# Performance work log

Measured on AMD Instinct MI355X. Metric: run time of the kernel, lower is better.

## Reference

```python
import jax, jax.numpy as jnp
import numpy as np

B, T, D, H = 1, 2048, 1024, 16
Dh = D // H
GSA_SCALE = 0.25
LN_EPS = 1e-5


def setup_inputs() -> dict:
    key = jax.random.key(0)
    ks = jax.random.split(key, 24)
    s = 0.02
    def W(k, din, dout):
        return jax.random.normal(k, (din, dout), jnp.float32) * s
    inp = dict(
        x=jax.random.normal(ks[0], (B, T, D), jnp.float32),
        mask=jnp.ones((B, T, T), jnp.bool_),
        # MultiHeadAttention params (linears[0..3] = q,k,v,o)
        mha_wq=W(ks[1], D, D), mha_bq=jnp.zeros((D,), jnp.float32),
        mha_wk=W(ks[2], D, D), mha_bk=jnp.zeros((D,), jnp.float32),
        mha_wv=W(ks[3], D, D), mha_bv=jnp.zeros((D,), jnp.float32),
        mha_wo=W(ks[4], D, D), mha_bo=jnp.zeros((D,), jnp.float32),
        # _GeodesicSelfAttention params
        gsa_wq=W(ks[5], D, D), gsa_bq=jnp.zeros((D,), jnp.float32),
        gsa_wk=W(ks[6], D, D), gsa_bk=jnp.zeros((D,), jnp.float32),
        gsa_wv=W(ks[7], D, D), gsa_bv=jnp.zeros((D,), jnp.float32),
        gsa_wo=W(ks[8], D, D), gsa_bo=jnp.zeros((D,), jnp.float32),
        log_diag=jnp.zeros((H, Dh), jnp.float32),  # nn.Parameter(torch.zeros(h, dk))
        # LayerNorms
        ln_mha_g=jnp.ones((D,), jnp.float32), ln_mha_b=jnp.zeros((D,), jnp.float32),
        ln_gsa_g=jnp.ones((D,), jnp.float32), ln_gsa_b=jnp.zeros((D,), jnp.float32),
        # mix scalar (initialized to -2.0 in __init__)
        gsa_mix=jnp.asarray(-2.0, jnp.float32),
        # gate: Linear(D,D) -> GELU -> Linear(D,1), last bias filled with 0.5
        gate_w1=W(ks[9], D, D), gate_b1=jnp.zeros((D,), jnp.float32),
        gate_w2=W(ks[10], D, 1), gate_b2=jnp.full((1,), 0.5, jnp.float32),
    )
    return inp


def _ln(x, g, b):
    m = x.mean(-1, keepdims=True)
    v = ((x - m) ** 2).mean(-1, keepdims=True)
    return (x - m) / jnp.sqrt(v + LN_EPS) * g + b


def _heads(y):  # [B,T,D] -> [B,H,T,Dh]
    return y.reshape(B, T, H, Dh).transpose(0, 2, 1, 3)


def _merge(y):  # [B,H,T,Dh] -> [B,T,D]
    return y.transpose(0, 2, 1, 3).reshape(B, T, D)


def _forward(x, mask, mha_wq, mha_bq, mha_wk, mha_bk, mha_wv, mha_bv, mha_wo, mha_bo,
             gsa_wq, gsa_bq, gsa_wk, gsa_bk, gsa_wv, gsa_bv, gsa_wo, gsa_bo,
             log_diag, ln_mha_g, ln_mha_b, ln_gsa_g, ln_gsa_b, gsa_mix,
             gate_w1, gate_b1, gate_w2, gate_b2):
    inv_sqrt_dh = 1.0 / jnp.sqrt(jnp.float32(Dh))
    m4 = mask[:, None, :, :]  # [B,1,T,T]

    # ---- standard MHA branch ----
    q = _heads(x @ mha_wq + mha_bq)
    k = _heads(x @ mha_wk + mha_bk)
    v = _heads(x @ mha_wv + mha_bv)
    scores = jnp.einsum('bhtd,bhsd->bhts', q, k) * inv_sqrt_dh
    scores = jnp.where(m4, scores, -jnp.inf)
    p = jax.nn.softmax(scores, axis=-1)
    mha_out = _merge(jnp.einsum('bhts,bhsd->bhtd', p, v)) @ mha_wo + mha_bo

    # ---- geodesic (Mahalanobis) branch ----
    qg = _heads(x @ gsa_wq + gsa_bq)
    kg = _heads(x @ gsa_wk + gsa_bk)
    vg = _heads(x @ gsa_wv + gsa_bv)
    diag = jax.nn.softplus(log_diag) + 1e-6          # [H,Dh]
    diag4 = diag[None, :, None, :]
    qM = qg * diag4
    q2M = (qg * qM).sum(-1)                           # [B,H,T]
    k2M = (kg * (kg * diag4)).sum(-1)                 # [B,H,T]
    cross = jnp.einsum('bhtd,bhsd->bhts', qM, kg)     # [B,H,T,T]
    dist = q2M[..., :, None] + k2M[..., None, :] - 2.0 * cross
    s = -0.5 * dist * inv_sqrt_dh
    s = jnp.where(m4, s, -jnp.inf)
    all_inf = jnp.all(jnp.isneginf(s), axis=-1, keepdims=True)
    s = jnp.where(all_inf, 0.0, s)
    pg = jax.nn.softmax(s * GSA_SCALE, axis=-1)
    gsa_out = _merge(jnp.einsum('bhts,bhsd->bhtd', pg, vg)) @ gsa_wo + gsa_bo

    # ---- gated mix ----
    mha_out = _ln(mha_out, ln_mha_g, ln_mha_b)
    gsa_out = jax.nn.sigmoid(gsa_mix) * _ln(gsa_out, ln_gsa_g, ln_gsa_b)
    g = jax.nn.gelu(x @ gate_w1 + gate_b1, approximate=False) @ gate_w2 + gate_b2
    alpha = 0.9 * jax.nn.sigmoid(g)                   # alpha_cap = 0.9, [B,T,1]
    return alpha * mha_out + (1.0 - alpha) * gsa_out


def reference(x, mask, mha_wq, mha_bq, mha_wk, mha_bk, mha_wv, mha_bv, mha_wo, mha_bo,
              gsa_wq, gsa_bq, gsa_wk, gsa_bk, gsa_wv, gsa_bv, gsa_wo, gsa_bo,
              log_diag, ln_mha_g, ln_mha_b, ln_gsa_g, ln_gsa_b, gsa_mix,
              gate_w1, gate_b1, gate_w2, gate_b2):
    return _forward(x, mask, mha_wq, mha_bq, mha_wk, mha_bk, mha_wv, mha_bv, mha_wo, mha_bo,
                    gsa_wq, gsa_bq, gsa_wk, gsa_bk, gsa_wv, gsa_bv, gsa_wo, gsa_bo,
                    log_diag, ln_mha_g, ln_mha_b, ln_gsa_g, ln_gsa_b, gsa_mix,
                    gate_w1, gate_b1, gate_w2, gate_b2)
```

## Files before the change

### kernel.cpp

```cpp
#include <hip/hip_runtime.h>
#include <stdint.h>

typedef unsigned short u16;
typedef u16   u16x4  __attribute__((ext_vector_type(4)));
typedef u16   u16x8  __attribute__((ext_vector_type(8)));
typedef __bf16 bf16x8 __attribute__((ext_vector_type(8)));
typedef float f32x4  __attribute__((ext_vector_type(4)));

#define SEQ   2048
#define DM    1024
#define NHEAD 16
#define DHEAD 64

#define QM_SCALE 0.180336880f
#define QG_SCALE 0.045084220f
#define K2_SCALE 0.022542110f

static __device__ __forceinline__ u16 f2b(float f) {
  uint32_t u = __float_as_uint(f);
  u += 0x7fffu + ((u >> 16) & 1u);
  return (u16)(u >> 16);
}
static __device__ __forceinline__ float b2f(u16 u) {
  return __uint_as_float(((uint32_t)u) << 16);
}

static __device__ __forceinline__ void gload16(const u16* g, u16* l) {
  __builtin_amdgcn_global_load_lds(
      (const __attribute__((address_space(1))) unsigned int*)g,
      (__attribute__((address_space(3))) unsigned int*)l, 16, 0, 0);
}

__global__ void precast_kernel(const float* __restrict__ x, u16* __restrict__ xb,
                               const float* __restrict__ log_diag, float* __restrict__ diag) {
  int i = blockIdx.x * 256 + threadIdx.x;
  if (i < SEQ * DM) xb[i] = f2b(x[i]);
  if (i < NHEAD * DHEAD) {
    float v = log_diag[i];
    float sp = (v > 20.f) ? v : log1pf(__expf(v));
    diag[i] = sp + 1e-6f;
  }
}

struct WTArgs { const float* w[9]; u16* o[9]; };

__global__ __launch_bounds__(256) void wtrans_kernel(WTArgs a) {
  const float* __restrict__ src = a.w[blockIdx.z];
  u16* __restrict__ dst = a.o[blockIdx.z];
  int r0 = blockIdx.y * 64, c0 = blockIdx.x * 64;
  __shared__ float tile[64][65];
  int tid = threadIdx.x;
  int r = tid >> 2, o8 = (tid & 3) * 16;
#pragma unroll
  for (int i = 0; i < 16; i += 4) {
    float4 v = *(const float4*)&src[(r0 + r) * DM + c0 + o8 + i];
    tile[r][o8 + i + 0] = v.x; tile[r][o8 + i + 1] = v.y;
    tile[r][o8 + i + 2] = v.z; tile[r][o8 + i + 3] = v.w;
  }
  __syncthreads();
  u16x8 w0, w1;
#pragma unroll
  for (int i = 0; i < 8; ++i) w0[i] = f2b(tile[o8 + i][r]);
#pragma unroll
  for (int i = 0; i < 8; ++i) w1[i] = f2b(tile[o8 + 8 + i][r]);
  *(u16x8*)&dst[(c0 + r) * DM + r0 + o8]     = w0;
  *(u16x8*)&dst[(c0 + r) * DM + r0 + o8 + 8] = w1;
}

struct GemmDesc { const u16* A; const u16* Bt; const float* bias; void* out;
                  int mode; int k0; int klen; float scale; };
struct GemmParams { GemmDesc d[8]; const float* diag; };

__global__ __launch_bounds__(256) void gemm_bt_kernel(GemmParams p) {
  GemmDesc g = p.d[blockIdx.z];
  const int K = DM;
  const int m0 = blockIdx.y * 128, n0 = blockIdx.x * 128;
  const int tid = threadIdx.x;
  const int wave = tid >> 6, lane = tid & 63, ln = lane & 15, quad = lane >> 4;
  const int wr = (wave >> 1) * 64, wc = (wave & 1) * 64;

  __shared__ __align__(16) u16 As[2 * 128 * 32];
  __shared__ __align__(16) u16 Bs[2 * 128 * 32];

  const f32x4 fz = {0.f, 0.f, 0.f, 0.f};
  f32x4 acc[4][4];
#pragma unroll
  for (int i = 0; i < 4; ++i)
#pragma unroll
    for (int j = 0; j < 4; ++j) acc[i][j] = fz;

  const u16* Aps[4]; const u16* Bps[4]; u16* dstA[4]; u16* dstB[4];
#pragma unroll
  for (int s = 0; s < 4; ++s) {
    int vr = s * 64 + wave * 16 + (lane >> 2);
    int c = vr >> 7, row = vr & 127;
    Aps[s] = g.A  + (size_t)(m0 + row) * K + g.k0 + c * 32 + (lane & 3) * 8;
    Bps[s] = g.Bt + (size_t)(n0 + row) * K + g.k0 + c * 32 + (lane & 3) * 8;
    dstA[s] = &As[s * 2048 + tid * 8];
    dstB[s] = &Bs[s * 2048 + tid * 8];
  }

  for (int kk = 0; kk < g.klen; kk += 64) {
#pragma unroll
    for (int s = 0; s < 4; ++s) {
      gload16(Aps[s] + kk, dstA[s]);
      gload16(Bps[s] + kk, dstB[s]);
    }
    __syncthreads();
#pragma unroll
    for (int c = 0; c < 2; ++c) {
      bf16x8 af[4], bfr[4];
#pragma unroll
      for (int mb = 0; mb < 4; ++mb)
        af[mb] = *(const bf16x8*)&As[c * 4096 + (wr + mb * 16 + ln) * 32 + quad * 8];
#pragma unroll
      for (int nb = 0; nb < 4; ++nb)
        bfr[nb] = *(const bf16x8*)&Bs[c * 4096 + (wc + nb * 16 + ln) * 32 + quad * 8];
#pragma unroll
      for (int mb = 0; mb < 4; ++mb)
#pragma unroll
        for (int nb = 0; nb < 4; ++nb)
          acc[mb][nb] = __builtin_amdgcn_mfma_f32_16x16x32_bf16(af[mb], bfr[nb], acc[mb][nb], 0, 0, 0);
    }
    __syncthreads();
  }

  const int mode = g.mode;
#pragma unroll
  for (int mb = 0; mb < 4; ++mb) {
    int row = m0 + wr + mb * 16 + quad * 4;
#pragma unroll
    for (int nb = 0; nb < 4; ++nb) {
      int col = n0 + wc + nb * 16 + ln;
      float bv = g.bias ? g.bias[col] : 0.f;
      f32x4 a = acc[mb][nb];
#pragma unroll
      for (int r = 0; r < 4; ++r) {
        float v = a[r] + bv;
        int rw = row + r;
        if (mode == 0) {
          ((u16*)g.out)[((size_t)(col >> 6) * SEQ + rw) * DHEAD + (col & 63)] = f2b(v);
        } else if (mode == 1) {
          ((u16*)g.out)[((size_t)(col >> 6) * SEQ + rw) * DHEAD + (col & 63)] = f2b(v * g.scale);
        } else if (mode == 2) {
          ((u16*)g.out)[((size_t)(col >> 6) * SEQ + rw) * DHEAD + (col & 63)] = f2b(v * p.diag[col] * g.scale);
        } else if (mode == 3) {
          v = 0.5f * v * (1.f + erff(v * 0.70710678f));
          ((u16*)g.out)[(size_t)rw * DM + col] = f2b(v);
        } else {
          ((float*)g.out)[(size_t)rw * DM + col] = v;
        }
      }
    }
  }
}

__global__ void k2m_kernel(const u16* __restrict__ Kg, const float* __restrict__ diag,
                           float* __restrict__ k2m) {
  int gr = blockIdx.x * 4 + (threadIdx.x >> 6);
  int lane = threadIdx.x & 63;
  float kv = b2f(Kg[(size_t)gr * 64 + lane]);
  int h = gr >> 11;
  float v = kv * kv * diag[h * 64 + lane];
#pragma unroll
  for (int d = 32; d >= 1; d >>= 1) v += __shfl_xor(v, d);
  if (lane == 0) k2m[gr] = v * K2_SCALE;
}

__global__ __launch_bounds__(256) void vtrans_kernel(const u16* __restrict__ Vm, u16* __restrict__ VmT,
                                                     const u16* __restrict__ Vg, u16* __restrict__ VgT) {
  const u16* __restrict__ src = blockIdx.z ? Vg : Vm;
  u16* __restrict__ dst = blockIdx.z ? VgT : VmT;
  int h = blockIdx.y, t0 = blockIdx.x * 64;
  __shared__ u16 tile[64][72];
  int tid = threadIdx.x;
  int r = tid >> 2, o16 = (tid & 3) * 16;
  *(u16x8*)&tile[r][o16]     = *(const u16x8*)&src[((size_t)(h * SEQ) + t0 + r) * 64 + o16];
  *(u16x8*)&tile[r][o16 + 8] = *(const u16x8*)&src[((size_t)(h * SEQ) + t0 + r) * 64 + o16 + 8];
  __syncthreads();
  u16x8 w0, w1;
#pragma unroll
  for (int i = 0; i < 8; ++i) w0[i] = tile[o16 + i][r];
#pragma unroll
  for (int i = 0; i < 8; ++i) w1[i] = tile[o16 + 8 + i][r];
  *(u16x8*)&dst[((size_t)(h * 64) + r) * SEQ + t0 + o16]     = w0;
  *(u16x8*)&dst[((size_t)(h * 64) + r) * SEQ + t0 + o16 + 8] = w1;
}

__global__ __launch_bounds__(256) void flash_kernel(
    const u16* __restrict__ Qm, const u16* __restrict__ Km, const u16* __restrict__ VmT,
    const u16* __restrict__ Qg, const u16* __restrict__ Kg, const u16* __restrict__ VgT,
    const float* __restrict__ k2m, u16* __restrict__ attM, u16* __restrict__ attG) {
  const int z = blockIdx.z;
  const u16* __restrict__ Q  = z ? Qg  : Qm;
  const u16* __restrict__ Kp = z ? Kg  : Km;
  const u16* __restrict__ Vt = z ? VgT : VmT;
  u16* __restrict__ out = z ? attG : attM;
  const int h = blockIdx.y;
  const int tid = threadIdx.x, wave = tid >> 6, lane = tid & 63, ln = lane & 15, quad = lane >> 4;
  const int wrow = blockIdx.x * 64 + wave * 16;

  __shared__ __align__(16) u16 Ks[64 * 72];
  __shared__ __align__(16) u16 Vs[80 * 72];
  __shared__ __align__(16) u16 Pt[4][16 * 72];
  __shared__ float k2s[64];

  bf16x8 qf[2];
#pragma unroll
  for (int kb = 0; kb < 2; ++kb)
    qf[kb] = *(const bf16x8*)&Q[((size_t)(h * SEQ) + wrow + ln) * 64 + kb * 32 + quad * 8];

  const f32x4 fz = {0.f, 0.f, 0.f, 0.f};
  f32x4 o[5];
#pragma unroll
  for (int db = 0; db < 5; ++db) o[db] = fz;

  const int sr = tid >> 2, sc = (tid & 3) * 16;
  const u16* Kbase = Kp + (size_t)h * SEQ * 64;
  const u16* Vbase = Vt + (size_t)h * 64 * SEQ;

  if (tid < 36) ((uint32_t*)&Vs[64 * 72])[tid] = 0x3F803F80u;

  u16x8 kr0 = *(const u16x8*)&Kbase[(size_t)sr * 64 + sc];
  u16x8 kr1 = *(const u16x8*)&Kbase[(size_t)sr * 64 + sc + 8];
  u16x8 vr0 = *(const u16x8*)&Vbase[(size_t)sr * SEQ + sc];
  u16x8 vr1 = *(const u16x8*)&Vbase[(size_t)sr * SEQ + sc + 8];
  float k2r = 0.f;
  if (z && tid < 64) k2r = k2m[h * SEQ + tid];

  for (int kt = 0; kt < SEQ; kt += 64) {
    *(u16x8*)&Ks[sr * 72 + sc]     = kr0;
    *(u16x8*)&Ks[sr * 72 + sc + 8] = kr1;
    *(u16x8*)&Vs[sr * 72 + sc]     = vr0;
    *(u16x8*)&Vs[sr * 72 + sc + 8] = vr1;
    if (z && tid < 64) k2s[tid] = k2r;
    __syncthreads();
    if (kt + 64 < SEQ) {
      kr0 = *(const u16x8*)&Kbase[(size_t)(kt + 64 + sr) * 64 + sc];
      kr1 = *(const u16x8*)&Kbase[(size_t)(kt + 64 + sr) * 64 + sc + 8];
      vr0 = *(const u16x8*)&Vbase[(size_t)sr * SEQ + kt + 64 + sc];
      vr1 = *(const u16x8*)&Vbase[(size_t)sr * SEQ + kt + 64 + sc + 8];
      if (z && tid < 64) k2r = k2m[h * SEQ + kt + 64 + tid];
    }

    f32x4 st[4];
#pragma unroll
    for (int sb = 0; sb < 4; ++sb) {
      st[sb] = fz;
      bf16x8 kf0 = *(const bf16x8*)&Ks[(sb * 16 + ln) * 72 + quad * 8];
      bf16x8 kf1 = *(const bf16x8*)&Ks[(sb * 16 + ln) * 72 + 32 + quad * 8];
      st[sb] = __builtin_amdgcn_mfma_f32_16x16x32_bf16(kf0, qf[0], st[sb], 0, 0, 0);
      st[sb] = __builtin_amdgcn_mfma_f32_16x16x32_bf16(kf1, qf[1], st[sb], 0, 0, 0);
    }

#pragma unroll
    for (int sb = 0; sb < 4; ++sb) {
      if (z) {
        f32x4 b4 = *(const f32x4*)&k2s[sb * 16 + quad * 4];
#pragma unroll
        for (int r = 0; r < 4; ++r) st[sb][r] -= b4[r];
      }
      uint32_t eb[4];
#pragma unroll
      for (int r = 0; r < 4; ++r)
        eb[r] = __float_as_uint(__builtin_amdgcn_exp2f(st[sb][r]));
      uint32_t lo = __builtin_amdgcn_perm(eb[1], eb[0], 0x07060302u);
      uint32_t hi = __builtin_amdgcn_perm(eb[3], eb[2], 0x07060302u);
      uint2 pk = {lo, hi};
      *(uint2*)&Pt[wave][ln * 72 + sb * 16 + quad * 4] = pk;
    }
    __asm__ __volatile__("" ::: "memory");

    bf16x8 pf0 = *(const bf16x8*)&Pt[wave][ln * 72 + quad * 8];
    bf16x8 pf1 = *(const bf16x8*)&Pt[wave][ln * 72 + 32 + quad * 8];
#pragma unroll
    for (int db = 0; db < 5; ++db) {
      bf16x8 vf0 = *(const bf16x8*)&Vs[(db * 16 + ln) * 72 + quad * 8];
      bf16x8 vf1 = *(const bf16x8*)&Vs[(db * 16 + ln) * 72 + 32 + quad * 8];
      o[db] = __builtin_amdgcn_mfma_f32_16x16x32_bf16(vf0, pf0, o[db], 0, 0, 0);
      o[db] = __builtin_amdgcn_mfma_f32_16x16x32_bf16(vf1, pf1, o[db], 0, 0, 0);
    }
    __syncthreads();
  }

  float l_all = __shfl(o[4][0], ln);
  float inv = 1.f / l_all;
#pragma unroll
  for (int db = 0; db < 4; ++db) {
    u16x4 w;
#pragma unroll
    for (int r = 0; r < 4; ++r) w[r] = f2b(o[db][r] * inv);
    *(u16x4*)&out[(size_t)(wrow + ln) * DM + h * 64 + db * 16 + quad * 4] = w;
  }
}

__global__ __launch_bounds__(256) void final_kernel(
    const float* __restrict__ p0, const float* __restrict__ p1,
    const float* __restrict__ p2, const float* __restrict__ p3,
    const u16* __restrict__ G1, const float* __restrict__ w2,
    const float* __restrict__ b2, const float* __restrict__ mixp,
    const float* __restrict__ gm, const float* __restrict__ bm,
    const float* __restrict__ gg, const float* __restrict__ bg,
    float* __restrict__ out) {
  int t = blockIdx.x, tid = threadIdx.x;
  float xm[4], xg[4];
  float sm = 0.f, sm2 = 0.f, sg = 0.f, sg2 = 0.f, sd = 0.f;
#pragma unroll
  for (int j0 = 0; j0 < 4; ++j0) {
    int j = tid + j0 * 256;
    size_t idx = (size_t)t * DM + j;
    float a = p0[idx] + p1[idx];
    float b = p2[idx] + p3[idx];
    xm[j0] = a; xg[j0] = b;
    sm += a; sm2 += a * a; sg += b; sg2 += b * b;
    sd += b2f(G1[idx]) * w2[j];
  }
#pragma unroll
  for (int d = 32; d >= 1; d >>= 1) {
    sm += __shfl_xor(sm, d); sm2 += __shfl_xor(sm2, d);
    sg += __shfl_xor(sg, d); sg2 += __shfl_xor(sg2, d);
    sd += __shfl_xor(sd, d);
  }
  __shared__ float red[5][4];
  int wave = tid >> 6;
  if ((tid & 63) == 0) {
    red[0][wave] = sm; red[1][wave] = sm2; red[2][wave] = sg;
    red[3][wave] = sg2; red[4][wave] = sd;
  }
  __syncthreads();
  sm  = red[0][0] + red[0][1] + red[0][2] + red[0][3];
  sm2 = red[1][0] + red[1][1] + red[1][2] + red[1][3];
  sg  = red[2][0] + red[2][1] + red[2][2] + red[2][3];
  sg2 = red[3][0] + red[3][1] + red[3][2] + red[3][3];
  sd  = red[4][0] + red[4][1] + red[4][2] + red[4][3];

  float mm = sm / DM, vm = fmaxf(sm2 / DM - mm * mm, 0.f);
  float rm = rsqrtf(vm + 1e-5f);
  float mg = sg / DM, vg = fmaxf(sg2 / DM - mg * mg, 0.f);
  float rg = rsqrtf(vg + 1e-5f);
  float alpha = 0.9f / (1.f + __expf(-(sd + b2[0])));
  float mix = 1.f / (1.f + __expf(-mixp[0]));
#pragma unroll
  for (int j0 = 0; j0 < 4; ++j0) {
    int j = tid + j0 * 256;
    float lm = (xm[j0] - mm) * rm * gm[j] + bm[j];
    float lg = (xg[j0] - mg) * rg * gg[j] + bg[j];
    out[(size_t)t * DM + j] = alpha * lm + (1.f - alpha) * mix * lg;
  }
}

extern "C" void kernel_launch(void* const* d_in, const int* in_sizes, int n_in,
                              void* d_out, int out_size, void* d_ws, size_t ws_size,
                              hipStream_t stream) {
  const float* x        = (const float*)d_in[0];
  const float* mha_wq = (const float*)d_in[2];
  const float* mha_bq = (const float*)d_in[3];
  const float* mha_wk = (const float*)d_in[4];
  const float* mha_bk = (const float*)d_in[5];
  const float* mha_wv = (const float*)d_in[6];
  const float* mha_bv = (const float*)d_in[7];
  const float* mha_wo = (const float*)d_in[8];
  const float* mha_bo = (const float*)d_in[9];
  const float* gsa_wq = (const float*)d_in[10];
  const float* gsa_bq = (const float*)d_in[11];
  const float* gsa_wk = (const float*)d_in[12];
  const float* gsa_bk = (const float*)d_in[13];
  const float* gsa_wv = (const float*)d_in[14];
  const float* gsa_bv = (const float*)d_in[15];
  const float* gsa_wo = (const float*)d_in[16];
  const float* gsa_bo = (const float*)d_in[17];
  const float* log_diag = (const float*)d_in[18];
  const float* ln_mha_g = (const float*)d_in[19];
  const float* ln_mha_b = (const float*)d_in[20];
  const float* ln_gsa_g = (const float*)d_in[21];
  const float* ln_gsa_b = (const float*)d_in[22];
  const float* gsa_mix  = (const float*)d_in[23];
  const float* gate_w1  = (const float*)d_in[24];
  const float* gate_b1  = (const float*)d_in[25];
  const float* gate_w2  = (const float*)d_in[26];
  const float* gate_b2  = (const float*)d_in[27];

  char* ws = (char*)d_ws;
  size_t off = 0;
  auto alloc = [&](size_t bytes) -> void* {
    void* p = ws + off;
    off += (bytes + 255) & ~(size_t)255;
    return p;
  };

  u16* xb = (u16*)alloc((size_t)SEQ * DM * 2);
  u16* wT[9];
  for (int i = 0; i < 9; ++i) wT[i] = (u16*)alloc((size_t)DM * DM * 2);
  float* diag = (float*)alloc((size_t)DM * 4);
  u16* Qm  = (u16*)alloc((size_t)SEQ * DM * 2);
  u16* Km  = (u16*)alloc((size_t)SEQ * DM * 2);
  u16* Vm  = (u16*)alloc((size_t)SEQ * DM * 2);
  u16* VmT = (u16*)alloc((size_t)SEQ * DM * 2);
  u16* Qg  = (u16*)alloc((size_t)SEQ * DM * 2);
  u16* Kg  = (u16*)alloc((size_t)SEQ * DM * 2);
  u16* Vg  = (u16*)alloc((size_t)SEQ * DM * 2);
  u16* VgT = (u16*)alloc((size_t)SEQ * DM * 2);
  float* k2m = (float*)alloc((size_t)NHEAD * SEQ * 4);
  u16* G1   = (u16*)alloc((size_t)SEQ * DM * 2);
  u16* attM = (u16*)alloc((size_t)SEQ * DM * 2);
  u16* attG = (u16*)alloc((size_t)SEQ * DM * 2);
  float* proj0 = (float*)Qm;
  float* proj1 = proj0 + (size_t)SEQ * DM;
  float* proj2 = proj1 + (size_t)SEQ * DM;
  float* proj3 = proj2 + (size_t)SEQ * DM;

  precast_kernel<<<(SEQ * DM) / 256, 256, 0, stream>>>(x, xb, log_diag, diag);

  WTArgs wa;
  wa.w[0] = mha_wq; wa.w[1] = mha_wk; wa.w[2] = mha_wv; wa.w[3] = mha_wo;
  wa.w[4] = gsa_wq; wa.w[5] = gsa_wk; wa.w[6] = gsa_wv; wa.w[7] = gsa_wo;
  wa.w[8] = gate_w1;
  for (int i = 0; i < 9; ++i) wa.o[i] = wT[i];
  wtrans_kernel<<<dim3(16, 16, 9), 256, 0, stream>>>(wa);

  GemmParams gp{};
  gp.diag = diag;
  gp.d[0] = {xb, wT[0], mha_bq, (void*)Qm, 1, 0, DM, QM_SCALE};
  gp.d[1] = {xb, wT[1], mha_bk, (void*)Km, 0, 0, DM, 1.f};
  gp.d[2] = {xb, wT[2], mha_bv, (void*)Vm, 0, 0, DM, 1.f};
  gp.d[3] = {xb, wT[4], gsa_bq, (void*)Qg, 2, 0, DM, QG_SCALE};
  gp.d[4] = {xb, wT[5], gsa_bk, (void*)Kg, 0, 0, DM, 1.f};
  gp.d[5] = {xb, wT[6], gsa_bv, (void*)Vg, 0, 0, DM, 1.f};
  gp.d[6] = {xb, wT[8], gate_b1, (void*)G1, 3, 0, DM, 1.f};
  gemm_bt_kernel<<<dim3(8, 16, 7), 256, 0, stream>>>(gp);

  k2m_kernel<<<(NHEAD * SEQ) / 4, 256, 0, stream>>>(Kg, diag, k2m);
  vtrans_kernel<<<dim3(SEQ / 64, NHEAD, 2), 256, 0, stream>>>(Vm, VmT, Vg, VgT);
  flash_kernel<<<dim3(SEQ / 64, NHEAD, 2), 256, 0, stream>>>(Qm, Km, VmT, Qg, Kg, VgT, k2m, attM, attG);

  GemmParams gp2{};
  gp2.diag = diag;
  gp2.d[0] = {attM, wT[3], mha_bo, (void*)proj0, 4, 0,   512, 1.f};
  gp2.d[1] = {attM, wT[3], nullptr, (void*)proj1, 4, 512, 512, 1.f};
  gp2.d[2] = {attG, wT[7], gsa_bo, (void*)proj2, 4, 0,   512, 1.f};
  gp2.d[3] = {attG, wT[7], nullptr, (void*)proj3, 4, 512, 512, 1.f};
  gemm_bt_kernel<<<dim3(8, 16, 4), 256, 0, stream>>>(gp2);

  final_kernel<<<SEQ, 256, 0, stream>>>(proj0, proj1, proj2, proj3, G1,
                                        gate_w2, gate_b2, gsa_mix,
                                        ln_mha_g, ln_mha_b, ln_gsa_g, ln_gsa_b,
                                        (float*)d_out);
}
```

Baseline: 328.7 us.

## Fuse V transpose and K-norm into GEMM epilogue, merge prep kernels, narrow GEMM tiles

Merges the x cast and diag softplus into the weight-transpose launch, and shrinks GEMM tiles to 128x64 so each block covers exactly one head. The QKV GEMM epilogue now writes V already transposed and computes the diag-weighted squared key norms in place. This removes the separate vtrans and k2m kernels and their extra passes over memory. Narrower tiles double the block count but lower per-block reuse, and the transposed stores are strided.

```diff
diff --git a/kernel.cpp b/kernel.cpp
--- a/kernel.cpp
+++ b/kernel.cpp
@@ -31,25 +31,35 @@
       (__attribute__((address_space(3))) unsigned int*)l, 16, 0, 0);
 }
 
-__global__ void precast_kernel(const float* __restrict__ x, u16* __restrict__ xb,
-                               const float* __restrict__ log_diag, float* __restrict__ diag) {
-  int i = blockIdx.x * 256 + threadIdx.x;
-  if (i < SEQ * DM) xb[i] = f2b(x[i]);
-  if (i < NHEAD * DHEAD) {
-    float v = log_diag[i];
-    float sp = (v > 20.f) ? v : log1pf(__expf(v));
-    diag[i] = sp + 1e-6f;
-  }
-}
-
-struct WTArgs { const float* w[9]; u16* o[9]; };
-
-__global__ __launch_bounds__(256) void wtrans_kernel(WTArgs a) {
-  const float* __restrict__ src = a.w[blockIdx.z];
-  u16* __restrict__ dst = a.o[blockIdx.z];
+struct PrepArgs { const float* w[9]; u16* o[9];
+                  const float* x; u16* xb; const float* log_diag; float* diag; };
+
+__global__ __launch_bounds__(256) void prep_kernel(PrepArgs a) {
+  const int z = blockIdx.z, tid = threadIdx.x;
+  if (z == 9) {
+    int b = blockIdx.y * 16 + blockIdx.x;
+#pragma unroll
+    for (int j = 0; j < 8; ++j) {
+      int idx = b * 8192 + j * 1024 + tid * 4;
+      float4 v = *(const float4*)&a.x[idx];
+      u16x4 w = {f2b(v.x), f2b(v.y), f2b(v.z), f2b(v.w)};
+      *(u16x4*)&a.xb[idx] = w;
+    }
+    if (b == 0) {
+#pragma unroll
+      for (int j = 0; j < 4; ++j) {
+        int i = j * 256 + tid;
+        float v = a.log_diag[i];
+        float sp = (v > 20.f) ? v : log1pf(__expf(v));
+        a.diag[i] = sp + 1e-6f;
+      }
+    }
+    return;
+  }
+  const float* __restrict__ src = a.w[z];
+  u16* __restrict__ dst = a.o[z];
   int r0 = blockIdx.y * 64, c0 = blockIdx.x * 64;
   __shared__ float tile[64][65];
-  int tid = threadIdx.x;
   int r = tid >> 2, o8 = (tid & 3) * 16;
 #pragma unroll
   for (int i = 0; i < 16; i += 4) {
@@ -68,56 +78,55 @@
 }
 
 struct GemmDesc { const u16* A; const u16* Bt; const float* bias; void* out;
-                  int mode; int k0; int klen; float scale; };
+                  float* aux; int mode; int k0; int klen; float scale; };
 struct GemmParams { GemmDesc d[8]; const float* diag; };
 
 __global__ __launch_bounds__(256) void gemm_bt_kernel(GemmParams p) {
   GemmDesc g = p.d[blockIdx.z];
   const int K = DM;
-  const int m0 = blockIdx.y * 128, n0 = blockIdx.x * 128;
+  const int m0 = blockIdx.y * 128, n0 = blockIdx.x * 64;
   const int tid = threadIdx.x;
   const int wave = tid >> 6, lane = tid & 63, ln = lane & 15, quad = lane >> 4;
-  const int wr = (wave >> 1) * 64, wc = (wave & 1) * 64;
 
   __shared__ __align__(16) u16 As[2 * 128 * 32];
-  __shared__ __align__(16) u16 Bs[2 * 128 * 32];
+  __shared__ __align__(16) u16 Bs[2 * 64 * 32];
 
   const f32x4 fz = {0.f, 0.f, 0.f, 0.f};
-  f32x4 acc[4][4];
-#pragma unroll
-  for (int i = 0; i < 4; ++i)
+  f32x4 acc[2][4];
+#pragma unroll
+  for (int i = 0; i < 2; ++i)
 #pragma unroll
     for (int j = 0; j < 4; ++j) acc[i][j] = fz;
 
-  const u16* Aps[4]; const u16* Bps[4]; u16* dstA[4]; u16* dstB[4];
+  const u16* Aps[4]; const u16* Bps[2];
 #pragma unroll
   for (int s = 0; s < 4; ++s) {
-    int vr = s * 64 + wave * 16 + (lane >> 2);
-    int c = vr >> 7, row = vr & 127;
-    Aps[s] = g.A  + (size_t)(m0 + row) * K + g.k0 + c * 32 + (lane & 3) * 8;
-    Bps[s] = g.Bt + (size_t)(n0 + row) * K + g.k0 + c * 32 + (lane & 3) * 8;
-    dstA[s] = &As[s * 2048 + tid * 8];
-    dstB[s] = &Bs[s * 2048 + tid * 8];
+    int vr = s * 64 + (tid >> 2);
+    Aps[s] = g.A + (size_t)(m0 + (vr & 127)) * K + g.k0 + (vr >> 7) * 32 + (tid & 3) * 8;
+  }
+#pragma unroll
+  for (int s = 0; s < 2; ++s) {
+    int vr = s * 64 + (tid >> 2);
+    Bps[s] = g.Bt + (size_t)(n0 + (vr & 63)) * K + g.k0 + (vr >> 6) * 32 + (tid & 3) * 8;
   }
 
   for (int kk = 0; kk < g.klen; kk += 64) {
 #pragma unroll
-    for (int s = 0; s < 4; ++s) {
-      gload16(Aps[s] + kk, dstA[s]);
-      gload16(Bps[s] + kk, dstB[s]);
-    }
+    for (int s = 0; s < 4; ++s) gload16(Aps[s] + kk, &As[s * 2048 + tid * 8]);
+#pragma unroll
+    for (int s = 0; s < 2; ++s) gload16(Bps[s] + kk, &Bs[s * 2048 + tid * 8]);
     __syncthreads();
 #pragma unroll
     for (int c = 0; c < 2; ++c) {
-      bf16x8 af[4], bfr[4];
-#pragma unroll
-      for (int mb = 0; mb < 4; ++mb)
-        af[mb] = *(const bf16x8*)&As[c * 4096 + (wr + mb * 16 + ln) * 32 + quad * 8];
+      bf16x8 af[2], bfr[4];
+#pragma unroll
+      for (int mb = 0; mb < 2; ++mb)
+        af[mb] = *(const bf16x8*)&As[(c * 128 + wave * 32 + mb * 16 + ln) * 32 + quad * 8];
 #pragma unroll
       for (int nb = 0; nb < 4; ++nb)
-        bfr[nb] = *(const bf16x8*)&Bs[c * 4096 + (wc + nb * 16 + ln) * 32 + quad * 8];
-#pragma unroll
-      for (int mb = 0; mb < 4; ++mb)
+        bfr[nb] = *(const bf16x8*)&Bs[(c * 64 + nb * 16 + ln) * 32 + quad * 8];
+#pragma unroll
+      for (int mb = 0; mb < 2; ++mb)
 #pragma unroll
         for (int nb = 0; nb < 4; ++nb)
           acc[mb][nb] = __builtin_amdgcn_mfma_f32_16x16x32_bf16(af[mb], bfr[nb], acc[mb][nb], 0, 0, 0);
@@ -126,65 +135,54 @@
   }
 
   const int mode = g.mode;
-#pragma unroll
-  for (int mb = 0; mb < 4; ++mb) {
-    int row = m0 + wr + mb * 16 + quad * 4;
+  const int h = n0 >> 6;
+#pragma unroll
+  for (int mb = 0; mb < 2; ++mb) {
+    int row = m0 + wave * 32 + mb * 16 + quad * 4;
+    float ksum[4] = {0.f, 0.f, 0.f, 0.f};
 #pragma unroll
     for (int nb = 0; nb < 4; ++nb) {
-      int col = n0 + wc + nb * 16 + ln;
+      int col = n0 + nb * 16 + ln;
       float bv = g.bias ? g.bias[col] : 0.f;
       f32x4 a = acc[mb][nb];
+      if (mode == 5) {
+        u16x4 w;
+#pragma unroll
+        for (int r = 0; r < 4; ++r) w[r] = f2b(a[r] + bv);
+        *(u16x4*)&((u16*)g.out)[((size_t)(h * 64) + nb * 16 + ln) * SEQ + row] = w;
+        continue;
+      }
 #pragma unroll
       for (int r = 0; r < 4; ++r) {
         float v = a[r] + bv;
         int rw = row + r;
         if (mode == 0) {
-          ((u16*)g.out)[((size_t)(col >> 6) * SEQ + rw) * DHEAD + (col & 63)] = f2b(v);
+          ((u16*)g.out)[((size_t)h * SEQ + rw) * DHEAD + (col & 63)] = f2b(v);
         } else if (mode == 1) {
-          ((u16*)g.out)[((size_t)(col >> 6) * SEQ + rw) * DHEAD + (col & 63)] = f2b(v * g.scale);
+          ((u16*)g.out)[((size_t)h * SEQ + rw) * DHEAD + (col & 63)] = f2b(v * g.scale);
         } else if (mode == 2) {
-          ((u16*)g.out)[((size_t)(col >> 6) * SEQ + rw) * DHEAD + (col & 63)] = f2b(v * p.diag[col] * g.scale);
+          ((u16*)g.out)[((size_t)h * SEQ + rw) * DHEAD + (col & 63)] = f2b(v * p.diag[col] * g.scale);
         } else if (mode == 3) {
-          v = 0.5f * v * (1.f + erff(v * 0.70710678f));
-          ((u16*)g.out)[(size_t)rw * DM + col] = f2b(v);
+          float gg = 0.5f * v * (1.f + erff(v * 0.70710678f));
+          ((u16*)g.out)[(size_t)rw * DM + col] = f2b(gg);
+        } else if (mode == 4) {
+          ((float*)g.out)[(size_t)rw * DM + col] = v;
         } else {
-          ((float*)g.out)[(size_t)rw * DM + col] = v;
+          ((u16*)g.out)[((size_t)h * SEQ + rw) * DHEAD + (col & 63)] = f2b(v);
+          ksum[r] += v * v * p.diag[col];
         }
       }
     }
-  }
-}
-
-__global__ void k2m_kernel(const u16* __restrict__ Kg, const float* __restrict__ diag,
-                           float* __restrict__ k2m) {
-  int gr = blockIdx.x * 4 + (threadIdx.x >> 6);
-  int lane = threadIdx.x & 63;
-  float kv = b2f(Kg[(size_t)gr * 64 + lane]);
-  int h = gr >> 11;
-  float v = kv * kv * diag[h * 64 + lane];
-#pragma unroll
-  for (int d = 32; d >= 1; d >>= 1) v += __shfl_xor(v, d);
-  if (lane == 0) k2m[gr] = v * K2_SCALE;
-}
-
-__global__ __launch_bounds__(256) void vtrans_kernel(const u16* __restrict__ Vm, u16* __restrict__ VmT,
-                                                     const u16* __restrict__ Vg, u16* __restrict__ VgT) {
-  const u16* __restrict__ src = blockIdx.z ? Vg : Vm;
-  u16* __restrict__ dst = blockIdx.z ? VgT : VmT;
-  int h = blockIdx.y, t0 = blockIdx.x * 64;
-  __shared__ u16 tile[64][72];
-  int tid = threadIdx.x;
-  int r = tid >> 2, o16 = (tid & 3) * 16;
-  *(u16x8*)&tile[r][o16]     = *(const u16x8*)&src[((size_t)(h * SEQ) + t0 + r) * 64 + o16];
-  *(u16x8*)&tile[r][o16 + 8] = *(const u16x8*)&src[((size_t)(h * SEQ) + t0 + r) * 64 + o16 + 8];
-  __syncthreads();
-  u16x8 w0, w1;
-#pragma unroll
-  for (int i = 0; i < 8; ++i) w0[i] = tile[o16 + i][r];
-#pragma unroll
-  for (int i = 0; i < 8; ++i) w1[i] = tile[o16 + 8 + i][r];
-  *(u16x8*)&dst[((size_t)(h * 64) + r) * SEQ + t0 + o16]     = w0;
-  *(u16x8*)&dst[((size_t)(h * 64) + r) * SEQ + t0 + o16 + 8] = w1;
+    if (mode == 6) {
+#pragma unroll
+      for (int r = 0; r < 4; ++r) {
+        float s = ksum[r];
+        s += __shfl_xor(s, 1); s += __shfl_xor(s, 2);
+        s += __shfl_xor(s, 4); s += __shfl_xor(s, 8);
+        if (ln == 0) g.aux[(size_t)h * SEQ + row + r] = s * K2_SCALE;
+      }
+    }
+  }
 }
 
 __global__ __launch_bounds__(256) void flash_kernel(
@@ -394,52 +392,47 @@
   float* diag = (float*)alloc((size_t)DM * 4);
   u16* Qm  = (u16*)alloc((size_t)SEQ * DM * 2);
   u16* Km  = (u16*)alloc((size_t)SEQ * DM * 2);
-  u16* Vm  = (u16*)alloc((size_t)SEQ * DM * 2);
-  u16* VmT = (u16*)alloc((size_t)SEQ * DM * 2);
   u16* Qg  = (u16*)alloc((size_t)SEQ * DM * 2);
   u16* Kg  = (u16*)alloc((size_t)SEQ * DM * 2);
-  u16* Vg  = (u16*)alloc((size_t)SEQ * DM * 2);
+  u16* VmT = (u16*)alloc((size_t)SEQ * DM * 2);
   u16* VgT = (u16*)alloc((size_t)SEQ * DM * 2);
   float* k2m = (float*)alloc((size_t)NHEAD * SEQ * 4);
   u16* G1   = (u16*)alloc((size_t)SEQ * DM * 2);
   u16* attM = (u16*)alloc((size_t)SEQ * DM * 2);
   u16* attG = (u16*)alloc((size_t)SEQ * DM * 2);
+  float* proj3 = (float*)alloc((size_t)SEQ * DM * 4);
   float* proj0 = (float*)Qm;
-  float* proj1 = proj0 + (size_t)SEQ * DM;
-  float* proj2 = proj1 + (size_t)SEQ * DM;
-  float* proj3 = proj2 + (size_t)SEQ * DM;
-
-  precast_kernel<<<(SEQ * DM) / 256, 256, 0, stream>>>(x, xb, log_diag, diag);
-
-  WTArgs wa;
-  wa.w[0] = mha_wq; wa.w[1] = mha_wk; wa.w[2] = mha_wv; wa.w[3] = mha_wo;
-  wa.w[4] = gsa_wq; wa.w[5] = gsa_wk; wa.w[6] = gsa_wv; wa.w[7] = gsa_wo;
-  wa.w[8] = gate_w1;
-  for (int i = 0; i < 9; ++i) wa.o[i] = wT[i];
-  wtrans_kernel<<<dim3(16, 16, 9), 256, 0, stream>>>(wa);
+  float* proj1 = (float*)Qg;
+  float* proj2 = (float*)VmT;
+
+  PrepArgs pa;
+  pa.w[0] = mha_wq; pa.w[1] = mha_wk; pa.w[2] = mha_wv; pa.w[3] = mha_wo;
+  pa.w[4] = gsa_wq; pa.w[5] = gsa_wk; pa.w[6] = gsa_wv; pa.w[7] = gsa_wo;
+  pa.w[8] = gate_w1;
+  for (int i = 0; i < 9; ++i) pa.o[i] = wT[i];
+  pa.x = x; pa.xb = xb; pa.log_diag = log_diag; pa.diag = diag;
+  prep_kernel<<<dim3(16, 16, 10), 256, 0, stream>>>(pa);
 
   GemmParams gp{};
   gp.diag = diag;
-  gp.d[0] = {xb, wT[0], mha_bq, (void*)Qm, 1, 0, DM, QM_SCALE};
-  gp.d[1] = {xb, wT[1], mha_bk, (void*)Km, 0, 0, DM, 1.f};
-  gp.d[2] = {xb, wT[2], mha_bv, (void*)Vm, 0, 0, DM, 1.f};
-  gp.d[3] = {xb, wT[4], gsa_bq, (void*)Qg, 2, 0, DM, QG_SCALE};
-  gp.d[4] = {xb, wT[5], gsa_bk, (void*)Kg, 0, 0, DM, 1.f};
-  gp.d[5] = {xb, wT[6], gsa_bv, (void*)Vg, 0, 0, DM, 1.f};
-  gp.d[6] = {xb, wT[8], gate_b1, (void*)G1, 3, 0, DM, 1.f};
-  gemm_bt_kernel<<<dim3(8, 16, 7), 256, 0, stream>>>(gp);
-
-  k2m_kernel<<<(NHEAD * SEQ) / 4, 256, 0, stream>>>(Kg, diag, k2m);
-  vtrans_kernel<<<dim3(SEQ / 64, NHEAD, 2), 256, 0, stream>>>(Vm, VmT, Vg, VgT);
+  gp.d[0] = {xb, wT[0], mha_bq, (void*)Qm,  nullptr, 1, 0, DM, QM_SCALE};
+  gp.d[1] = {xb, wT[1], mha_bk, (void*)Km,  nullptr, 0, 0, DM, 1.f};
+  gp.d[2] = {xb, wT[2], mha_bv, (void*)VmT, nullptr, 5, 0, DM, 1.f};
+  gp.d[3] = {xb, wT[4], gsa_bq, (void*)Qg,  nullptr, 2, 0, DM, QG_SCALE};
+  gp.d[4] = {xb, wT[5], gsa_bk, (void*)Kg,  k2m,     6, 0, DM, 1.f};
+  gp.d[5] = {xb, wT[6], gsa_bv, (void*)VgT, nullptr, 5, 0, DM, 1.f};
+  gp.d[6] = {xb, wT[8], gate_b1,(void*)G1,  nullptr, 3, 0, DM, 1.f};
+  gemm_bt_kernel<<<dim3(16, 16, 7), 256, 0, stream>>>(gp);
+
   flash_kernel<<<dim3(SEQ / 64, NHEAD, 2), 256, 0, stream>>>(Qm, Km, VmT, Qg, Kg, VgT, k2m, attM, attG);
 
   GemmParams gp2{};
   gp2.diag = diag;
-  gp2.d[0] = {attM, wT[3], mha_bo, (void*)proj0, 4, 0,   512, 1.f};
-  gp2.d[1] = {attM, wT[3], nullptr, (void*)proj1, 4, 512, 512, 1.f};
-  gp2.d[2] = {attG, wT[7], gsa_bo, (void*)proj2, 4, 0,   512, 1.f};
-  gp2.d[3] = {attG, wT[7], nullptr, (void*)proj3, 4, 512, 512, 1.f};
-  gemm_bt_kernel<<<dim3(8, 16, 4), 256, 0, stream>>>(gp2);
+  gp2.d[0] = {attM, wT[3], mha_bo, (void*)proj0, nullptr, 4, 0,   512, 1.f};
+  gp2.d[1] = {attM, wT[3], nullptr,(void*)proj1, nullptr, 4, 512, 512, 1.f};
+  gp2.d[2] = {attG, wT[7], gsa_bo, (void*)proj2, nullptr, 4, 0,   512, 1.f};
+  gp2.d[3] = {attG, wT[7], nullptr,(void*)proj3, nullptr, 4, 512, 512, 1.f};
+  gemm_bt_kernel<<<dim3(16, 16, 4), 256, 0, stream>>>(gp2);
 
   final_kernel<<<SEQ, 256, 0, stream>>>(proj0, proj1, proj2, proj3, G1,
                                         gate_w2, gate_b2, gsa_mix,
```

Result: faster. 299.9 us (-8.8%).
